# Kernel tuning notes

Hardware: AMD Instinct MI355X
Metric: run time of the kernel (lower is better)

The kernel has to match this reference:

```python
import jax, jax.numpy as jnp
import numpy as np

N = 12288
E = 196608
H = 128
Z = 128
NEG = -1e9  # finite mask value (avoids -inf NaNs in grads)
WSCALE = 0.05


def setup_inputs() -> dict:
    key = jax.random.key(0)
    ks = jax.random.split(key, 16)
    inp = {}
    inp["x"] = jax.random.normal(ks[0], (N, 2), dtype=jnp.float32)
    inp["z"] = jax.random.normal(ks[1], (Z,), dtype=jnp.float32)
    inp["node_type"] = jax.random.randint(ks[2], (N,), 0, 3, dtype=jnp.int32)
    inp["node_depth"] = jax.random.randint(ks[3], (N,), 0, 64, dtype=jnp.int32)
    inp["edge_index"] = jax.random.randint(ks[4], (2, E), 0, N, dtype=jnp.int32)
    inp["W1"] = jax.random.normal(ks[5], (2, H), dtype=jnp.float32) * WSCALE
    inp["b1"] = jnp.zeros((H,), jnp.float32)
    inp["W2"] = jax.random.normal(ks[6], (H, H), dtype=jnp.float32) * WSCALE
    inp["b2"] = jnp.zeros((H,), jnp.float32)
    inp["Wm1"] = jax.random.normal(ks[7], (H + Z, H), dtype=jnp.float32) * WSCALE
    inp["bm1"] = jnp.zeros((H,), jnp.float32)
    inp["Wm2"] = jax.random.normal(ks[8], (H, H), dtype=jnp.float32) * WSCALE
    inp["bm2"] = jnp.zeros((H,), jnp.float32)
    inp["Ws"] = jax.random.normal(ks[9], (H, H), dtype=jnp.float32) * WSCALE
    inp["Wt"] = jax.random.normal(ks[10], (H, H), dtype=jnp.float32) * WSCALE
    inp["Wi1"] = jax.random.normal(ks[11], (2 * H + Z, H), dtype=jnp.float32) * WSCALE
    inp["bi1"] = jnp.zeros((H,), jnp.float32)
    inp["Wi2"] = jax.random.normal(ks[12], (H, 1), dtype=jnp.float32) * WSCALE
    inp["bi2"] = jnp.zeros((1,), jnp.float32)
    return inp


def _gcn(x, W, b, src, dst, n):
    # GCNConv with self-loops and symmetric deg^-1/2 normalization
    loop = jnp.arange(n, dtype=src.dtype)
    s = jnp.concatenate([src, loop])
    d = jnp.concatenate([dst, loop])
    deg = jax.ops.segment_sum(jnp.ones_like(d, dtype=x.dtype), d, num_segments=n)
    inv_sqrt = jnp.where(deg > 0, jax.lax.rsqrt(jnp.maximum(deg, 1.0)), 0.0)
    w = inv_sqrt[s] * inv_sqrt[d]  # [E+N]
    agg = jax.ops.segment_sum(x[s] * w[:, None], d, num_segments=n)  # [N,F]
    return agg @ W + b


def reference(x, z, node_type, node_depth, edge_index,
              W1, b1, W2, b2, Wm1, bm1, Wm2, bm2, Ws, Wt, Wi1, bi1, Wi2, bi2):
    n = x.shape[0]
    src, dst = edge_index[0], edge_index[1]
    # 2-layer GCN encode
    h = jax.nn.relu(_gcn(x, W1, b1, src, dst, n))
    h = jax.nn.relu(_gcn(h, W2, b2, src, dst, n))
    # node_mlp on [h, z] (no outer relu, per original edge_index branch)
    zb = jnp.broadcast_to(z, (n, Z))
    h = jax.nn.relu(jnp.concatenate([h, zb], axis=1) @ Wm1 + bm1) @ Wm2 + bm2  # [N,H]
    # batched score: St[v,u] = tgt_proj(h_v) . src_proj(h_u)
    St = (h @ Wt) @ (h @ Ws).T  # [N(target), N(candidate)]
    cand_ok = node_depth[None, :] < node_depth[:, None]  # candidate strictly shallower
    St = jnp.where(cand_ok, St, NEG)
    vals, idx = jax.lax.top_k(St, 2)  # [N,2] per-target top candidates
    # target is active if type != 0, depth > 0, and at least one candidate exists
    tv = (node_type != 0) & (node_depth > 0) & (vals[:, 0] > NEG / 2)
    # k=2 edges for AND nodes (type==2), else k=1
    edge_valid = jnp.stack([tv, tv & (node_type == 2)], axis=1)  # [N,2]
    # inversion bit mlp on [h_u, h_v, z]
    hu = h[idx]  # [N,2,H]
    hv = jnp.broadcast_to(h[:, None, :], hu.shape)
    zz = jnp.broadcast_to(z, (n, 2, Z))
    feat = jnp.concatenate([hu, hv, zz], axis=-1)  # [N,2,2H+Z]
    logit = (jax.nn.relu(feat @ Wi1 + bi1) @ Wi2 + bi2)[..., 0]  # [N,2]
    inv_prob = jax.nn.sigmoid(logit)
    return inv_prob, vals, idx, edge_valid
```

## Files before the change

kernel.cpp:

```cpp
#include <hip/hip_runtime.h>
#include <hip/hip_bf16.h>

#define NN 12288
#define NE 196608
#define HD 128
#define ZD 128
#define NEGV (-1.0e9f)
#define SEG 16

using s8v = __attribute__((ext_vector_type(8))) short;
using f4v = __attribute__((ext_vector_type(4))) float;
using i4v = __attribute__((ext_vector_type(4))) int;

__device__ __forceinline__ unsigned short f2bf(float f) {
    return __builtin_bit_cast(unsigned short, __float2bfloat16(f));
}
__device__ __forceinline__ float4 pack8(float4 a, float4 b) {
    unsigned p0 = ((unsigned)f2bf(a.y) << 16) | f2bf(a.x);
    unsigned p1 = ((unsigned)f2bf(a.w) << 16) | f2bf(a.z);
    unsigned p2 = ((unsigned)f2bf(b.y) << 16) | f2bf(b.x);
    unsigned p3 = ((unsigned)f2bf(b.w) << 16) | f2bf(b.z);
    i4v r = (i4v){(int)p0, (int)p1, (int)p2, (int)p3};
    return __builtin_bit_cast(float4, r);
}

__global__ __launch_bounds__(256) void k_counts_wz(
        const int* __restrict__ edst, const int* __restrict__ ndep,
        const float* __restrict__ W2, const float* __restrict__ Wm1,
        const float* __restrict__ Wm2, const float* __restrict__ Wtm,
        const float* __restrict__ Wsm, const float* __restrict__ Wi1,
        const float* __restrict__ z, const float* __restrict__ bm1,
        const float* __restrict__ bi1,
        int* degi, int* cnt, __hip_bfloat16* __restrict__ wt7,
        float* cz1, float* cz2) {
    __shared__ int lh[64];
    int tid = threadIdx.x;
    int bid = blockIdx.x;
    if (bid < NE / 256) {
        int e = bid * 256 + tid;
        atomicAdd(&degi[edst[e]], 1);
    } else if (bid < NE / 256 + NN / 256) {
        if (tid < 64) lh[tid] = 0;
        __syncthreads();
        int v = (bid - NE / 256) * 256 + tid;
        atomicAdd(&lh[ndep[v]], 1);
        __syncthreads();
        if (tid < 64) {
            int c = lh[tid];
            if (c) atomicAdd(&cnt[tid * 16], c);
        }
    } else if (bid < NE / 256 + NN / 256 + 448) {
        int flat = (bid - NE / 256 - NN / 256) * 256 + tid;
        int g = flat >> 14;
        int rem = flat & 16383;
        int k = rem >> 7, n = rem & 127;
        const float* src;
        if (g == 0) src = W2;
        else if (g == 1) src = Wm1;
        else if (g == 2) src = Wm2;
        else if (g == 3) src = Wtm;
        else if (g == 4) src = Wsm;
        else if (g == 5) src = Wi1;
        else src = Wi1 + 128 * HD;
        wt7[(g << 14) + n * 128 + k] = __float2bfloat16(src[rem]);
    } else {
        int j = tid & 127;
        const float* W = (tid < 128) ? (Wm1 + HD * HD) : (Wi1 + 2 * HD * HD);
        float A0 = 0.f, A1 = 0.f, A2 = 0.f, A3 = 0.f;
        for (int k = 0; k < ZD; k += 4) {
            A0 = fmaf(z[k],     W[(k    ) * HD + j], A0);
            A1 = fmaf(z[k + 1], W[(k + 1) * HD + j], A1);
            A2 = fmaf(z[k + 2], W[(k + 2) * HD + j], A2);
            A3 = fmaf(z[k + 3], W[(k + 3) * HD + j], A3);
        }
        float r = (A0 + A1) + (A2 + A3);
        if (tid < 128) cz1[j] = r + bm1[j];
        else           cz2[j] = r + bi1[j];
    }
}

__global__ __launch_bounds__(1024) void k_prefix(const int* __restrict__ degi,
                                                 const int* __restrict__ cnt,
                                                 const float* __restrict__ x,
                                                 float* inv, float* agg2,
                                                 int* offs, int* cursor,
                                                 int* bofs, int* dcur) {
    __shared__ int ldeg[NN];
    __shared__ int part[1024];
    __shared__ int stot;
    int tid = threadIdx.x;
#pragma unroll
    for (int k = 0; k < 12; ++k)
        ldeg[k * 1024 + tid] = degi[k * 1024 + tid];
    __syncthreads();
    int base = tid * 12;
    int s = 0;
#pragma unroll
    for (int k = 0; k < 12; ++k) s += ldeg[base + k];
    part[tid] = s;
    __syncthreads();
    for (int off = 1; off < 1024; off <<= 1) {
        int v = (tid >= off) ? part[tid - off] : 0;
        __syncthreads();
        part[tid] += v;
        __syncthreads();
    }
    int run = part[tid] - s;
#pragma unroll
    for (int k = 0; k < 12; ++k) {
        int d = ldeg[base + k];
        ldeg[base + k] = run;
        run += d;
    }
    if (tid == 1023) stot = run;
    __syncthreads();
    int total = stot;
    const float2* X2 = (const float2*)x;
    float2* A2 = (float2*)agg2;
#pragma unroll
    for (int k = 0; k < 12; ++k) {
        int i = k * 1024 + tid;
        int p = ldeg[i];
        int nxt = (i < NN - 1) ? ldeg[i + 1] : total;
        int d = nxt - p;
        offs[i] = p;
        cursor[i] = p;
        float iv = rsqrtf((float)(d + 1));
        inv[i] = iv;
        float w = iv * iv;
        float2 xv = X2[i];
        float2 av; av.x = xv.x * w; av.y = xv.y * w;
        A2[i] = av;
    }
    if (tid == 0) {
        offs[NN] = total;
        int r = 0;
        for (int d = 0; d < 64; ++d) {
            bofs[d] = r;
            dcur[d * 16] = r;
            r += cnt[d * 16];
        }
        bofs[64] = r;
    }
}

__global__ __launch_bounds__(256) void k_bucket_scatter(
        const int* __restrict__ esrc, const int* __restrict__ edst,
        const int* __restrict__ ndep, const float* __restrict__ inv,
        int* cursor, int* ebsrc, float* ebw,
        int* dcur, int* sidx, int* sdep, int* prank) {
    __shared__ int lh[64];
    __shared__ int lbase[64];
    int tid = threadIdx.x;
    if (blockIdx.x < NE / 256) {
        int e = blockIdx.x * 256 + tid;
        int u = esrc[e], v = edst[e];
        int pos = atomicAdd(&cursor[v], 1);
        ebsrc[pos] = u;
        ebw[pos] = inv[u] * inv[v];
    } else {
        if (tid < 64) lh[tid] = 0;
        __syncthreads();
        int v = (blockIdx.x - NE / 256) * 256 + tid;
        int d = ndep[v];
        int r = atomicAdd(&lh[d], 1);
        __syncthreads();
        if (tid < 64) {
            int c = lh[tid];
            if (c) lbase[tid] = atomicAdd(&dcur[tid * 16], c);
        }
        __syncthreads();
        int p = lbase[d] + r;
        sidx[p] = v;
        sdep[p] = d;
        prank[v] = p;
    }
}

__global__ __launch_bounds__(256) void k_gl1(const int* __restrict__ offs,
                                             const int* __restrict__ ebsrc,
                                             const float* __restrict__ ebw,
                                             const float* __restrict__ x,
                                             const float* __restrict__ agg2,
                                             const float* __restrict__ W1,
                                             const float* __restrict__ b1,
                                             const float* __restrict__ inv,
                                             unsigned short* h1b, float* aggH) {
    __shared__ float2 la[32];
    int tid = threadIdx.x;
    int v0 = blockIdx.x * 32;
    {
        int nb = tid >> 3;
        int sl = tid & 7;
        int v = v0 + nb;
        int b = offs[v], e = offs[v + 1];
        const float2* X2 = (const float2*)x;
        float ax = 0.f, ay = 0.f;
        for (int k = b + sl; k < e; k += 8) {
            int u = ebsrc[k];
            float w = ebw[k];
            float2 xv = X2[u];
            ax = fmaf(xv.x, w, ax);
            ay = fmaf(xv.y, w, ay);
        }
#pragma unroll
        for (int m = 1; m < 8; m <<= 1) {
            ax += __shfl_xor(ax, m, 64);
            ay += __shfl_xor(ay, m, 64);
        }
        if (sl == 0) {
            float2 seed = ((const float2*)agg2)[v];
            seed.x += ax; seed.y += ay;
            la[nb] = seed;
        }
    }
    __syncthreads();
    {
#pragma unroll
        for (int k = 0; k < 16; ++k) {
            int idx = k * 256 + tid;
            int vloc = idx >> 7, j = idx & 127;
            float2 a = la[vloc];
            float hv = fmaxf(fmaf(a.x, W1[j], fmaf(a.y, W1[HD + j], b1[j])), 0.f);
            int t = (v0 + vloc) * HD + j;
            h1b[t] = f2bf(hv);
            float iv = inv[v0 + vloc];
            aggH[t] = hv * iv * iv;
        }
    }
}

__global__ __launch_bounds__(256) void k_gatherH(const int* __restrict__ offs,
                                                 const int* __restrict__ ebsrc,
                                                 const float* __restrict__ ebw,
                                                 const unsigned short* __restrict__ h1b,
                                                 float* aggH) {
    int tid = threadIdx.x;
    int lane = tid & 63;
    int v = blockIdx.x * 4 + (tid >> 6);
    const unsigned* H1 = (const unsigned*)h1b;
    float2* A2 = (float2*)aggH;
    float2 acc = A2[(size_t)v * 64 + lane];
    int b = offs[v], e = offs[v + 1];
    int k = b;
    for (; k + 4 <= e; k += 4) {
        int u0 = ebsrc[k], u1 = ebsrc[k + 1], u2 = ebsrc[k + 2], u3 = ebsrc[k + 3];
        float w0 = ebw[k], w1 = ebw[k + 1], w2 = ebw[k + 2], w3 = ebw[k + 3];
        unsigned hb0 = H1[(size_t)u0 * 64 + lane];
        unsigned hb1 = H1[(size_t)u1 * 64 + lane];
        unsigned hb2 = H1[(size_t)u2 * 64 + lane];
        unsigned hb3 = H1[(size_t)u3 * 64 + lane];
        acc.x = fmaf(__builtin_bit_cast(float, hb0 << 16), w0, acc.x);
        acc.y = fmaf(__builtin_bit_cast(float, hb0 & 0xFFFF0000u), w0, acc.y);
        acc.x = fmaf(__builtin_bit_cast(float, hb1 << 16), w1, acc.x);
        acc.y = fmaf(__builtin_bit_cast(float, hb1 & 0xFFFF0000u), w1, acc.y);
        acc.x = fmaf(__builtin_bit_cast(float, hb2 << 16), w2, acc.x);
        acc.y = fmaf(__builtin_bit_cast(float, hb2 & 0xFFFF0000u), w2, acc.y);
        acc.x = fmaf(__builtin_bit_cast(float, hb3 << 16), w3, acc.x);
        acc.y = fmaf(__builtin_bit_cast(float, hb3 & 0xFFFF0000u), w3, acc.y);
    }
    for (; k < e; ++k) {
        int u = ebsrc[k];
        float w = ebw[k];
        unsigned hb = H1[(size_t)u * 64 + lane];
        acc.x = fmaf(__builtin_bit_cast(float, hb << 16), w, acc.x);
        acc.y = fmaf(__builtin_bit_cast(float, hb & 0xFFFF0000u), w, acc.y);
    }
    A2[(size_t)v * 64 + lane] = acc;
}

#define AFRAGS(BUF) \
    s8v a0_ = __builtin_bit_cast(s8v, (BUF)[lane16 * 16 + ((quad     ) ^ lane16)]); \
    s8v a1_ = __builtin_bit_cast(s8v, (BUF)[lane16 * 16 + ((quad +  4) ^ lane16)]); \
    s8v a2_ = __builtin_bit_cast(s8v, (BUF)[lane16 * 16 + ((quad +  8) ^ lane16)]); \
    s8v a3_ = __builtin_bit_cast(s8v, (BUF)[lane16 * 16 + ((quad + 12) ^ lane16)]);

#define NBACC(WT4, NCOL, ACC) \
    f4v ACC = (f4v){0.f, 0.f, 0.f, 0.f}; \
    ACC = __builtin_amdgcn_mfma_f32_16x16x32_bf16(a0_, __builtin_bit_cast(s8v, (WT4)[(NCOL) * 16 + quad     ]), ACC, 0, 0, 0); \
    ACC = __builtin_amdgcn_mfma_f32_16x16x32_bf16(a1_, __builtin_bit_cast(s8v, (WT4)[(NCOL) * 16 + quad +  4]), ACC, 0, 0, 0); \
    ACC = __builtin_amdgcn_mfma_f32_16x16x32_bf16(a2_, __builtin_bit_cast(s8v, (WT4)[(NCOL) * 16 + quad +  8]), ACC, 0, 0, 0); \
    ACC = __builtin_amdgcn_mfma_f32_16x16x32_bf16(a3_, __builtin_bit_cast(s8v, (WT4)[(NCOL) * 16 + quad + 12]), ACC, 0, 0, 0);

#define BST(EXPR, RR, COL, USPTR) { int rw_ = quad * 4 + (RR); int cc_ = (COL) >> 3; \
    (USPTR)[rw_ * 128 + (((cc_ ^ rw_)) << 3) + ((COL) & 7)] = f2bf(EXPR); }

#define LDS4R(ACC, B, COL, US) \
    BST(fmaxf(ACC[0] + (B), 0.f), 0, COL, US) BST(fmaxf(ACC[1] + (B), 0.f), 1, COL, US) \
    BST(fmaxf(ACC[2] + (B), 0.f), 2, COL, US) BST(fmaxf(ACC[3] + (B), 0.f), 3, COL, US)

#define LDS4(ACC, B, COL, US) \
    BST(ACC[0] + (B), 0, COL, US) BST(ACC[1] + (B), 1, COL, US) \
    BST(ACC[2] + (B), 2, COL, US) BST(ACC[3] + (B), 3, COL, US)

#define GBF4S(ACC, COL, PTR) \
    ((unsigned short*)(PTR))[(size_t)pr0 * HD + (COL)] = f2bf(ACC[0]); \
    ((unsigned short*)(PTR))[(size_t)pr1 * HD + (COL)] = f2bf(ACC[1]); \
    ((unsigned short*)(PTR))[(size_t)pr2 * HD + (COL)] = f2bf(ACC[2]); \
    ((unsigned short*)(PTR))[(size_t)pr3 * HD + (COL)] = f2bf(ACC[3]);

#define GF4(ACC, B, COL, PTR) \
    (PTR)[(size_t)(r0 + quad * 4 + 0) * HD + (COL)] = ACC[0] + (B); \
    (PTR)[(size_t)(r0 + quad * 4 + 1) * HD + (COL)] = ACC[1] + (B); \
    (PTR)[(size_t)(r0 + quad * 4 + 2) * HD + (COL)] = ACC[2] + (B); \
    (PTR)[(size_t)(r0 + quad * 4 + 3) * HD + (COL)] = ACC[3] + (B);

__global__ __launch_bounds__(256) void k_mlp7_mfma(
        const float* __restrict__ s1in, const __hip_bfloat16* __restrict__ wt7,
        const float* __restrict__ bb2, const float* __restrict__ bcz1,
        const float* __restrict__ bbm2, const float* __restrict__ bcz2,
        const int* __restrict__ prank,
        float* __restrict__ outA, float* __restrict__ outB,
        __hip_bfloat16* __restrict__ htb, __hip_bfloat16* __restrict__ hsb) {
    __shared__ float4 bufA4[256];
    __shared__ float4 bufB4[256];
    int tid = threadIdx.x;
    int wv = tid >> 6;
    int l = tid & 63;
    int lane16 = l & 15;
    int quad = l >> 4;
    int r0 = blockIdx.x * 16;
    const float4* wt4 = (const float4*)wt7;

    int pr0 = prank[r0 + quad * 4 + 0];
    int pr1 = prank[r0 + quad * 4 + 1];
    int pr2 = prank[r0 + quad * 4 + 2];
    int pr3 = prank[r0 + quad * 4 + 3];

    {
        const float4* g4 = (const float4*)(s1in + (size_t)r0 * HD);
        float4 u0 = g4[2 * tid], u1 = g4[2 * tid + 1];
        int row_ = tid >> 4, c_ = tid & 15;
        bufA4[row_ * 16 + (c_ ^ row_)] = pack8(u0, u1);
    }
    __syncthreads();
    int col0 = wv * 32 + lane16, col1 = col0 + 16;
    unsigned short* usA = (unsigned short*)bufA4;
    unsigned short* usB = (unsigned short*)bufB4;

    {
        AFRAGS(bufA4)
        NBACC(wt4, col0, cA) NBACC(wt4, col1, cB)
        float q0 = bb2[col0], q1 = bb2[col1];
        LDS4R(cA, q0, col0, usB) LDS4R(cB, q1, col1, usB)
    }
    __syncthreads();
    {
        AFRAGS(bufB4)
        const float4* wt = wt4 + 2048;
        NBACC(wt, col0, cA) NBACC(wt, col1, cB)
        float q0 = bcz1[col0], q1 = bcz1[col1];
        LDS4R(cA, q0, col0, usA) LDS4R(cB, q1, col1, usA)
    }
    __syncthreads();
    {
        AFRAGS(bufA4)
        const float4* wt = wt4 + 2 * 2048;
        NBACC(wt, col0, cA) NBACC(wt, col1, cB)
        float q0 = bbm2[col0], q1 = bbm2[col1];
        LDS4(cA, q0, col0, usB) LDS4(cB, q1, col1, usB)
    }
    __syncthreads();
    {
        AFRAGS(bufB4)
        const float4* wt = wt4 + 3 * 2048;
        NBACC(wt, col0, cA) NBACC(wt, col1, cB)
        GBF4S(cA, col0, htb) GBF4S(cB, col1, htb)
    }
    {
        AFRAGS(bufB4)
        const float4* wt = wt4 + 4 * 2048;
        NBACC(wt, col0, cA) NBACC(wt, col1, cB)
        GBF4S(cA, col0, hsb) GBF4S(cB, col1, hsb)
    }
    {
        AFRAGS(bufB4)
        const float4* wt = wt4 + 5 * 2048;
        NBACC(wt, col0, cA) NBACC(wt, col1, cB)
        GF4(cA, 0.f, col0, outA) GF4(cB, 0.f, col1, outA)
    }
    {
        AFRAGS(bufB4)
        const float4* wt = wt4 + 6 * 2048;
        NBACC(wt, col0, cA) NBACC(wt, col1, cB)
        float q0 = bcz2[col0], q1 = bcz2[col1];
        GF4(cA, q0, col0, outB) GF4(cB, q1, col1, outB)
    }
}

#define STG(buf, q, val) { int r_ = (q) >> 4, c_ = (q) & 15; \
    (buf)[r_ * 16 + (c_ ^ (r_ & 7))] = (val); }

#define KC2(kc, AX, AY) { \
    int co_ = (kc) * 4 + quad; \
    int bo_ = bbase + (co_ ^ brm); \
    s8v b0_ = __builtin_bit_cast(s8v, B[bo_      ]); \
    s8v b1_ = __builtin_bit_cast(s8v, B[bo_ + 256]); \
    s8v b2_ = __builtin_bit_cast(s8v, B[bo_ + 512]); \
    s8v b3_ = __builtin_bit_cast(s8v, B[bo_ + 768]); \
    x0 = __builtin_amdgcn_mfma_f32_16x16x32_bf16(AX, b0_, x0, 0, 0, 0); \
    y0 = __builtin_amdgcn_mfma_f32_16x16x32_bf16(AY, b0_, y0, 0, 0, 0); \
    x1 = __builtin_amdgcn_mfma_f32_16x16x32_bf16(AX, b1_, x1, 0, 0, 0); \
    y1 = __builtin_amdgcn_mfma_f32_16x16x32_bf16(AY, b1_, y1, 0, 0, 0); \
    x2 = __builtin_amdgcn_mfma_f32_16x16x32_bf16(AX, b2_, x2, 0, 0, 0); \
    y2 = __builtin_amdgcn_mfma_f32_16x16x32_bf16(AY, b2_, y2, 0, 0, 0); \
    x3 = __builtin_amdgcn_mfma_f32_16x16x32_bf16(AX, b3_, x3, 0, 0, 0); \
    y3 = __builtin_amdgcn_mfma_f32_16x16x32_bf16(AY, b3_, y3, 0, 0, 0); }

#define RMG(K1, K2, EL, DV) { \
    unsigned pb_ = (__builtin_bit_cast(unsigned, EL) & 0xFFFFC000u) | e_; \
    float sf_ = __builtin_bit_cast(float, (du_ < (DV)) ? pb_ : negp_); \
    K2 = __builtin_amdgcn_fmed3f(K1, K2, sf_); \
    K1 = fmaxf(K1, sf_); }

#define MGEN(nb, XA, YA) { \
    unsigned pk_ = eds[ebase + (nb) * 16 + lane16]; \
    int du_ = (int)(pk_ >> 16); \
    unsigned e_ = pk_ & 0x3FFFu; \
    unsigned negp_ = negbase | e_; \
    RMG(k1x0, k2x0, XA[0], dvx0) RMG(k1x1, k2x1, XA[1], dvx1) \
    RMG(k1x2, k2x2, XA[2], dvx2) RMG(k1x3, k2x3, XA[3], dvx3) \
    RMG(k1y0, k2y0, YA[0], dvy0) RMG(k1y1, k2y1, YA[1], dvy1) \
    RMG(k1y2, k2y2, YA[2], dvy2) RMG(k1y3, k2y3, YA[3], dvy3) }

#define RMF(K1, K2, EL) { \
    float sf_ = __builtin_bit_cast(float, \
        (__builtin_bit_cast(unsigned, EL) & 0xFFFFC000u) | e_); \
    K2 = __builtin_amdgcn_fmed3f(K1, K2, sf_); \
    K1 = fmaxf(K1, sf_); }

#define MFAST(nb, XA, YA) { \
    unsigned e_ = eds[ebase + (nb) * 16 + lane16] & 0x3FFFu; \
    RMF(k1x0, k2x0, XA[0]) RMF(k1x1, k2x1, XA[1]) \
    RMF(k1x2, k2x2, XA[2]) RMF(k1x3, k2x3, XA[3]) \
    RMF(k1y0, k2y0, YA[0]) RMF(k1y1, k2y1, YA[1]) \
    RMF(k1y2, k2y2, YA[2]) RMF(k1y3, k2y3, YA[3]) }

#define BF1(K1, K2, m) { \
    float o1_ = __shfl_xor(K1, m, 64); \
    float o2_ = __shfl_xor(K2, m, 64); \
    float m2_ = fmaxf(K2, o2_); \
    K2 = __builtin_amdgcn_fmed3f(K1, o1_, m2_); \
    K1 = fmaxf(K1, o1_); }

#define BFALL(m) \
    BF1(k1x0, k2x0, m) BF1(k1x1, k2x1, m) BF1(k1x2, k2x2, m) BF1(k1x3, k2x3, m) \
    BF1(k1y0, k2y0, m) BF1(k1y1, k2y1, m) BF1(k1y2, k2y2, m) BF1(k1y3, k2y3, m)

#define EMIT2(K1, K2, GROW) { \
    size_t o = ((size_t)seg * NN + (GROW)) * 2; \
    pv[o] = K1; pv[o + 1] = K2; }

__global__ __launch_bounds__(256) void k_score_top2_mfma(
        const __hip_bfloat16* __restrict__ htb,
        const __hip_bfloat16* __restrict__ hsb,
        const int* __restrict__ sdep, const int* __restrict__ sidx,
        const int* __restrict__ bofs,
        float* __restrict__ pv) {
    __shared__ float4 Bs4[2][64 * 16];
    __shared__ unsigned eds[12 * 64];
    int tid = threadIdx.x;
    int w = tid >> 6;
    int l = tid & 63;
    int lane16 = l & 15;
    int quad = l >> 4;
    int rb = (int)gridDim.x - 1 - (int)blockIdx.x;
    int row0 = rb * 128;
    int seg = blockIdx.y;
    const unsigned negbase = __builtin_bit_cast(unsigned, NEGV) & 0xFFFFC000u;

    int dmax = sdep[row0 + 127];
    int lim = bofs[dmax];
    int nt = (lim + 63) >> 6;
    int ns = (nt + 11) / 12;
    if (ns < 1) ns = 1;
    if (seg >= ns) {
        if (tid < 128) {
            int grow = sidx[row0 + tid];
            size_t o = ((size_t)seg * NN + grow) * 2;
            pv[o]     = __builtin_bit_cast(float, negbase | 0x3FFFu);
            pv[o + 1] = __builtin_bit_cast(float, negbase | 0x3FFEu);
        }
        return;
    }
    int t0 = (seg * nt) / ns;
    int t1 = ((seg + 1) * nt) / ns;

    int rbase = row0 + w * 32;
    s8v ax0, ax1, ax2, ax3, ay0, ay1, ay2, ay3;
    {
        const float4* gx = (const float4*)(htb + (size_t)(rbase + lane16) * HD);
        ax0 = __builtin_bit_cast(s8v, gx[quad]);
        ax1 = __builtin_bit_cast(s8v, gx[4 + quad]);
        ax2 = __builtin_bit_cast(s8v, gx[8 + quad]);
        ax3 = __builtin_bit_cast(s8v, gx[12 + quad]);
        const float4* gy = (const float4*)(htb + (size_t)(rbase + 16 + lane16) * HD);
        ay0 = __builtin_bit_cast(s8v, gy[quad]);
        ay1 = __builtin_bit_cast(s8v, gy[4 + quad]);
        ay2 = __builtin_bit_cast(s8v, gy[8 + quad]);
        ay3 = __builtin_bit_cast(s8v, gy[12 + quad]);
    }
    for (int i = tid; i < (t1 - t0) * 64; i += 256) {
        int p = t0 * 64 + i;
        eds[i] = ((unsigned)sdep[p] << 16) | (0x3FFFu - (unsigned)sidx[p]);
    }
    if (t0 < t1) {
        float4* B0 = Bs4[t0 & 1];
        const float4* gb = (const float4*)(hsb + (size_t)(t0 * 64) * HD);
        float4 b0_ = gb[tid], b1_ = gb[tid + 256], b2_ = gb[tid + 512], b3_ = gb[tid + 768];
        STG(B0, tid, b0_) STG(B0, tid + 256, b1_)
        STG(B0, tid + 512, b2_) STG(B0, tid + 768, b3_)
    }

    int bbase = lane16 * 16, brm = lane16 & 7;

    int dvx0 = sdep[rbase + quad * 4 + 0];
    int dvx1 = sdep[rbase + quad * 4 + 1];
    int dvx2 = sdep[rbase + quad * 4 + 2];
    int dvx3 = sdep[rbase + quad * 4 + 3];
    int dvy0 = sdep[rbase + 16 + quad * 4 + 0];
    int dvy1 = sdep[rbase + 16 + quad * 4 + 1];
    int dvy2 = sdep[rbase + 16 + quad * 4 + 2];
    int dvy3 = sdep[rbase + 16 + quad * 4 + 3];
    int lim_lo = bofs[sdep[rbase]];
    int lim_hi = bofs[sdep[rbase + 31]];

    float ki1 = (lane16 == 0) ? __builtin_bit_cast(float, negbase | 0x3FFFu) : -3.4e38f;
    float ki2 = (lane16 == 0) ? __builtin_bit_cast(float, negbase | 0x3FFEu) : -3.4e38f;
    float k1x0 = ki1, k1x1 = ki1, k1x2 = ki1, k1x3 = ki1;
    float k1y0 = ki1, k1y1 = ki1, k1y2 = ki1, k1y3 = ki1;
    float k2x0 = ki2, k2x1 = ki2, k2x2 = ki2, k2x3 = ki2;
    float k2y0 = ki2, k2y1 = ki2, k2y2 = ki2, k2y3 = ki2;

    float4 p0, p1, p2, p3;
    for (int t = t0; t < t1; ++t) {
        int u0 = t * 64;
        int ebase = (t - t0) * 64;
        __syncthreads();
        if (t + 1 < t1) {
            const float4* g = (const float4*)(hsb + (size_t)(u0 + 64) * HD);
            p0 = g[tid]; p1 = g[tid + 256]; p2 = g[tid + 512]; p3 = g[tid + 768];
        }
        if (u0 < lim_hi) {
            const float4* B = Bs4[t & 1];
            f4v x0 = (f4v){0.f, 0.f, 0.f, 0.f};
            f4v x1 = (f4v){0.f, 0.f, 0.f, 0.f};
            f4v x2 = (f4v){0.f, 0.f, 0.f, 0.f};
            f4v x3 = (f4v){0.f, 0.f, 0.f, 0.f};
            f4v y0 = (f4v){0.f, 0.f, 0.f, 0.f};
            f4v y1 = (f4v){0.f, 0.f, 0.f, 0.f};
            f4v y2 = (f4v){0.f, 0.f, 0.f, 0.f};
            f4v y3 = (f4v){0.f, 0.f, 0.f, 0.f};
            KC2(0, ax0, ay0) KC2(1, ax1, ay1) KC2(2, ax2, ay2) KC2(3, ax3, ay3)
            if (u0 + 64 <= lim_lo) {
                MFAST(0, x0, y0) MFAST(1, x1, y1)
                MFAST(2, x2, y2) MFAST(3, x3, y3)
            } else {
                MGEN(0, x0, y0) MGEN(1, x1, y1)
                MGEN(2, x2, y2) MGEN(3, x3, y3)
            }
        }
        if (t + 1 < t1) {
            float4* Bn = Bs4[(t + 1) & 1];
            STG(Bn, tid, p0) STG(Bn, tid + 256, p1)
            STG(Bn, tid + 512, p2) STG(Bn, tid + 768, p3)
        }
    }

    BFALL(1) BFALL(2) BFALL(4) BFALL(8)

    if (lane16 == 0) {
        int gbse = rbase + quad * 4;
        EMIT2(k1x0, k2x0, sidx[gbse + 0])
        EMIT2(k1x1, k2x1, sidx[gbse + 1])
        EMIT2(k1x2, k2x2, sidx[gbse + 2])
        EMIT2(k1x3, k2x3, sidx[gbse + 3])
        EMIT2(k1y0, k2y0, sidx[gbse + 16])
        EMIT2(k1y1, k2y1, sidx[gbse + 17])
        EMIT2(k1y2, k2y2, sidx[gbse + 18])
        EMIT2(k1y3, k2y3, sidx[gbse + 19])
    }
}

__global__ __launch_bounds__(256) void k_final(const float* __restrict__ pv,
                                               const int* __restrict__ ntype,
                                               const int* __restrict__ ndepth,
                                               const float* __restrict__ A,
                                               const float* __restrict__ B,
                                               const float* __restrict__ Wi2,
                                               const float* __restrict__ bi2,
                                               float* __restrict__ out) {
    int tid = threadIdx.x;
    int lane = tid & 63;
    int v = blockIdx.x * 4 + (tid >> 6);

    float k1 = -3.4e38f;
    if (lane < 32) {
        k1 = pv[((size_t)(lane >> 1) * NN + v) * 2 + (lane & 1)];
    }
    float k2 = -3.4e38f;
#pragma unroll
    for (int m = 1; m <= 16; m <<= 1) {
        float o1 = __shfl_xor(k1, m, 64);
        float o2 = __shfl_xor(k2, m, 64);
        float m2 = fmaxf(k2, o2);
        k2 = __builtin_amdgcn_fmed3f(k1, o1, m2);
        k1 = fmaxf(k1, o1);
    }
    float K1 = __shfl(k1, 0, 64);
    float K2 = __shfl(k2, 0, 64);
    unsigned b1 = __builtin_bit_cast(unsigned, K1);
    unsigned b2 = __builtin_bit_cast(unsigned, K2);
    int I1 = 0x3FFF - (int)(b1 & 0x3FFFu);
    int I2 = 0x3FFF - (int)(b2 & 0x3FFFu);

    if (lane == 0) {
        int tp = ntype[v];
        bool tv = (tp != 0) && (ndepth[v] > 0) && (K1 > -5.0e8f);
        out[2 * NN + 2 * v]     = K1;
        out[2 * NN + 2 * v + 1] = K2;
        out[4 * NN + 2 * v]     = (float)I1;
        out[4 * NN + 2 * v + 1] = (float)I2;
        out[6 * NN + 2 * v]     = tv ? 1.f : 0.f;
        out[6 * NN + 2 * v + 1] = (tv && tp == 2) ? 1.f : 0.f;
    }

    int u1 = min(max(I1, 0), NN - 1);
    int u2 = min(max(I2, 0), NN - 1);
    const float2* A2p = (const float2*)A;
    float2 av1 = A2p[(size_t)u1 * 64 + lane];
    float2 av2 = A2p[(size_t)u2 * 64 + lane];
    float2 bv = ((const float2*)B)[(size_t)v * 64 + lane];
    float2 wv = ((const float2*)Wi2)[lane];
    float bias = bi2[0];
    float a1 = fmaf(fmaxf(av1.x + bv.x, 0.f), wv.x,
                    fmaxf(av1.y + bv.y, 0.f) * wv.y);
    float a2 = fmaf(fmaxf(av2.x + bv.x, 0.f), wv.x,
                    fmaxf(av2.y + bv.y, 0.f) * wv.y);
#pragma unroll
    for (int off = 32; off > 0; off >>= 1) {
        a1 += __shfl_down(a1, off);
        a2 += __shfl_down(a2, off);
    }
    if (lane == 0) {
        out[2 * v]     = 1.f / (1.f + expf(-(a1 + bias)));
        out[2 * v + 1] = 1.f / (1.f + expf(-(a2 + bias)));
    }
}

extern "C" void kernel_launch(void* const* d_in, const int* in_sizes, int n_in,
                              void* d_out, int out_size, void* d_ws, size_t ws_size,
                              hipStream_t stream) {
    (void)in_sizes; (void)n_in; (void)out_size; (void)ws_size;
    const float* x   = (const float*)d_in[0];
    const float* z   = (const float*)d_in[1];
    const int* ntype = (const int*)d_in[2];
    const int* ndep  = (const int*)d_in[3];
    const int* eidx  = (const int*)d_in[4];
    const float* W1  = (const float*)d_in[5];
    const float* b1  = (const float*)d_in[6];
    const float* W2  = (const float*)d_in[7];
    const float* b2  = (const float*)d_in[8];
    const float* Wm1 = (const float*)d_in[9];
    const float* bm1 = (const float*)d_in[10];
    const float* Wm2 = (const float*)d_in[11];
    const float* bm2 = (const float*)d_in[12];
    const float* Wsm = (const float*)d_in[13];
    const float* Wtm = (const float*)d_in[14];
    const float* Wi1 = (const float*)d_in[15];
    const float* bi1 = (const float*)d_in[16];
    const float* Wi2 = (const float*)d_in[17];
    const float* bi2 = (const float*)d_in[18];
    float* out = (float*)d_out;

    const int* esrc = eidx;
    const int* edst = eidx + NE;

    const size_t S2N = (size_t)SEG * 2 * NN;
    float* ws = (float*)d_ws;
    float* pv     = ws;
    int*   pi     = (int*)(pv + S2N);
    int*   cnt    = pi;
    int*   dcur   = pi + 1024;
    int*   degi   = pi + S2N;
    float* inv    = (float*)(degi + NN + 64);
    float* agg2   = inv + NN;
    float* cz1    = agg2 + 2 * NN;
    float* cz2    = cz1 + 128;
    int*   offs   = (int*)(cz2 + 128);
    int*   cursor = offs + NN + 16;
    int*   bofs   = cursor + NN;
    int*   sidx   = bofs + 80 + 64;
    int*   sdep   = sidx + NN;
    int*   prank  = sdep + NN;
    int*   ebsrc  = prank + NN;
    float* ebw    = (float*)(ebsrc + NE);
    __hip_bfloat16* wt7 = (__hip_bfloat16*)(ebw + NE);
    size_t F = (size_t)NN * HD;
    float* s0 = (float*)(wt7 + 7 * 16384);
    float* s1 = s0 + F;
    float* s2 = s1 + F;
    unsigned short* h1b = (unsigned short*)s0;
    __hip_bfloat16* htb = (__hip_bfloat16*)s0;
    __hip_bfloat16* hsb = htb + F;

    hipMemsetAsync(degi, 0, NN * sizeof(int), stream);
    hipMemsetAsync(cnt, 0, 1024 * sizeof(int), stream);
    k_counts_wz<<<NE / 256 + NN / 256 + 448 + 1, 256, 0, stream>>>(
        edst, ndep, W2, Wm1, Wm2, Wtm, Wsm, Wi1, z, bm1, bi1,
        degi, cnt, wt7, cz1, cz2);
    k_prefix<<<1, 1024, 0, stream>>>(degi, cnt, x, inv, agg2, offs, cursor, bofs, dcur);
    k_bucket_scatter<<<NE / 256 + NN / 256, 256, 0, stream>>>(
        esrc, edst, ndep, inv, cursor, ebsrc, ebw, dcur, sidx, sdep, prank);
    k_gl1<<<NN / 32, 256, 0, stream>>>(offs, ebsrc, ebw, x, agg2, W1, b1, inv,
                                       h1b, s1);
    k_gatherH<<<NN / 4, 256, 0, stream>>>(offs, ebsrc, ebw, h1b, s1);
    k_mlp7_mfma<<<NN / 16, 256, 0, stream>>>(s1, wt7, b2, cz1, bm2, cz2,
                                             prank, s2, s1, htb, hsb);
    k_score_top2_mfma<<<dim3(NN / 128, SEG), 256, 0, stream>>>(
        htb, hsb, sdep, sidx, bofs, pv);
    k_final<<<NN / 4, 256, 0, stream>>>(pv, ntype, ndep, s2, s1, Wi2, bi2, out);
}
```

Measured before the change: 225.6 us.

## Factor GCN edge weights into per-node scaling and transpose weights via shared memory

Removes the per-edge weight array by factoring the symmetric normalization: source features are pre-scaled by inv_sqrt (packed into an xi float4 and a pre-scaled bf16 h1), and the destination factor is applied once per node after the gather. This cuts the ebw writes in the scatter kernel and the ebw reads in both gather kernels. Separately, the weight transpose to bf16 now goes through a padded shared-memory tile, so both the reads and the writes are coalesced. In exchange the h1 values are rounded to bf16 after scaling, which shifts rounding slightly, and xi reuses the old ebw slot in the workspace.

```diff
diff --git a/kernel.cpp b/kernel.cpp
--- a/kernel.cpp
+++ b/kernel.cpp
@@ -34,6 +34,7 @@
         int* degi, int* cnt, __hip_bfloat16* __restrict__ wt7,
         float* cz1, float* cz2) {
     __shared__ int lh[64];
+    __shared__ float tl[16 * 129];
     int tid = threadIdx.x;
     int bid = blockIdx.x;
     if (bid < NE / 256) {
@@ -49,11 +50,10 @@
             int c = lh[tid];
             if (c) atomicAdd(&cnt[tid * 16], c);
         }
-    } else if (bid < NE / 256 + NN / 256 + 448) {
-        int flat = (bid - NE / 256 - NN / 256) * 256 + tid;
-        int g = flat >> 14;
-        int rem = flat & 16383;
-        int k = rem >> 7, n = rem & 127;
+    } else if (bid < NE / 256 + NN / 256 + 56) {
+        int b2 = bid - NE / 256 - NN / 256;
+        int g = b2 >> 3;
+        int k0 = (b2 & 7) << 4;
         const float* src;
         if (g == 0) src = W2;
         else if (g == 1) src = Wm1;
@@ -62,7 +62,19 @@
         else if (g == 4) src = Wsm;
         else if (g == 5) src = Wi1;
         else src = Wi1 + 128 * HD;
-        wt7[(g << 14) + n * 128 + k] = __float2bfloat16(src[rem]);
+#pragma unroll
+        for (int i = 0; i < 8; ++i) {
+            int idx = i * 256 + tid;
+            int kk = idx >> 7, n = idx & 127;
+            tl[kk * 129 + n] = src[(k0 + kk) * 128 + n];
+        }
+        __syncthreads();
+#pragma unroll
+        for (int i = 0; i < 8; ++i) {
+            int idx = i * 256 + tid;
+            int n = idx >> 4, kk = idx & 15;
+            wt7[(g << 14) + n * 128 + k0 + kk] = __float2bfloat16(tl[kk * 129 + n]);
+        }
     } else {
         int j = tid & 127;
         const float* W = (tid < 128) ? (Wm1 + HD * HD) : (Wi1 + 2 * HD * HD);
@@ -83,6 +95,7 @@
                                                  const int* __restrict__ cnt,
                                                  const float* __restrict__ x,
                                                  float* inv, float* agg2,
+                                                 float4* __restrict__ xi,
                                                  int* offs, int* cursor,
                                                  int* bofs, int* dcur) {
     __shared__ int ldeg[NN];
@@ -131,6 +144,8 @@
         float2 xv = X2[i];
         float2 av; av.x = xv.x * w; av.y = xv.y * w;
         A2[i] = av;
+        float4 xo; xo.x = xv.x; xo.y = xv.y; xo.z = iv; xo.w = 0.f;
+        xi[i] = xo;
     }
     if (tid == 0) {
         offs[NN] = total;
@@ -146,8 +161,8 @@
 
 __global__ __launch_bounds__(256) void k_bucket_scatter(
         const int* __restrict__ esrc, const int* __restrict__ edst,
-        const int* __restrict__ ndep, const float* __restrict__ inv,
-        int* cursor, int* ebsrc, float* ebw,
+        const int* __restrict__ ndep,
+        int* cursor, int* ebsrc,
         int* dcur, int* sidx, int* sdep, int* prank) {
     __shared__ int lh[64];
     __shared__ int lbase[64];
@@ -157,7 +172,6 @@
         int u = esrc[e], v = edst[e];
         int pos = atomicAdd(&cursor[v], 1);
         ebsrc[pos] = u;
-        ebw[pos] = inv[u] * inv[v];
     } else {
         if (tid < 64) lh[tid] = 0;
         __syncthreads();
@@ -179,8 +193,7 @@
 
 __global__ __launch_bounds__(256) void k_gl1(const int* __restrict__ offs,
                                              const int* __restrict__ ebsrc,
-                                             const float* __restrict__ ebw,
-                                             const float* __restrict__ x,
+                                             const float4* __restrict__ xi,
                                              const float* __restrict__ agg2,
                                              const float* __restrict__ W1,
                                              const float* __restrict__ b1,
@@ -194,14 +207,12 @@
         int sl = tid & 7;
         int v = v0 + nb;
         int b = offs[v], e = offs[v + 1];
-        const float2* X2 = (const float2*)x;
         float ax = 0.f, ay = 0.f;
         for (int k = b + sl; k < e; k += 8) {
             int u = ebsrc[k];
-            float w = ebw[k];
-            float2 xv = X2[u];
-            ax = fmaf(xv.x, w, ax);
-            ay = fmaf(xv.y, w, ay);
+            float4 xv = xi[u];
+            ax = fmaf(xv.x, xv.z, ax);
+            ay = fmaf(xv.y, xv.z, ay);
         }
 #pragma unroll
         for (int m = 1; m < 8; m <<= 1) {
@@ -209,8 +220,10 @@
             ay += __shfl_xor(ay, m, 64);
         }
         if (sl == 0) {
+            float ivv = inv[v];
             float2 seed = ((const float2*)agg2)[v];
-            seed.x += ax; seed.y += ay;
+            seed.x = fmaf(ax, ivv, seed.x);
+            seed.y = fmaf(ay, ivv, seed.y);
             la[nb] = seed;
         }
     }
@@ -223,8 +236,8 @@
             float2 a = la[vloc];
             float hv = fmaxf(fmaf(a.x, W1[j], fmaf(a.y, W1[HD + j], b1[j])), 0.f);
             int t = (v0 + vloc) * HD + j;
-            h1b[t] = f2bf(hv);
             float iv = inv[v0 + vloc];
+            h1b[t] = f2bf(hv * iv);
             aggH[t] = hv * iv * iv;
         }
     }
@@ -232,7 +245,7 @@
 
 __global__ __launch_bounds__(256) void k_gatherH(const int* __restrict__ offs,
                                                  const int* __restrict__ ebsrc,
-                                                 const float* __restrict__ ebw,
+                                                 const float* __restrict__ inv,
                                                  const unsigned short* __restrict__ h1b,
                                                  float* aggH) {
     int tid = threadIdx.x;
@@ -240,33 +253,35 @@
     int v = blockIdx.x * 4 + (tid >> 6);
     const unsigned* H1 = (const unsigned*)h1b;
     float2* A2 = (float2*)aggH;
-    float2 acc = A2[(size_t)v * 64 + lane];
+    float2 acc; acc.x = 0.f; acc.y = 0.f;
     int b = offs[v], e = offs[v + 1];
     int k = b;
     for (; k + 4 <= e; k += 4) {
         int u0 = ebsrc[k], u1 = ebsrc[k + 1], u2 = ebsrc[k + 2], u3 = ebsrc[k + 3];
-        float w0 = ebw[k], w1 = ebw[k + 1], w2 = ebw[k + 2], w3 = ebw[k + 3];
         unsigned hb0 = H1[(size_t)u0 * 64 + lane];
         unsigned hb1 = H1[(size_t)u1 * 64 + lane];
         unsigned hb2 = H1[(size_t)u2 * 64 + lane];
         unsigned hb3 = H1[(size_t)u3 * 64 + lane];
-        acc.x = fmaf(__builtin_bit_cast(float, hb0 << 16), w0, acc.x);
-        acc.y = fmaf(__builtin_bit_cast(float, hb0 & 0xFFFF0000u), w0, acc.y);
-        acc.x = fmaf(__builtin_bit_cast(float, hb1 << 16), w1, acc.x);
-        acc.y = fmaf(__builtin_bit_cast(float, hb1 & 0xFFFF0000u), w1, acc.y);
-        acc.x = fmaf(__builtin_bit_cast(float, hb2 << 16), w2, acc.x);
-        acc.y = fmaf(__builtin_bit_cast(float, hb2 & 0xFFFF0000u), w2, acc.y);
-        acc.x = fmaf(__builtin_bit_cast(float, hb3 << 16), w3, acc.x);
-        acc.y = fmaf(__builtin_bit_cast(float, hb3 & 0xFFFF0000u), w3, acc.y);
+        acc.x += __builtin_bit_cast(float, hb0 << 16);
+        acc.y += __builtin_bit_cast(float, hb0 & 0xFFFF0000u);
+        acc.x += __builtin_bit_cast(float, hb1 << 16);
+        acc.y += __builtin_bit_cast(float, hb1 & 0xFFFF0000u);
+        acc.x += __builtin_bit_cast(float, hb2 << 16);
+        acc.y += __builtin_bit_cast(float, hb2 & 0xFFFF0000u);
+        acc.x += __builtin_bit_cast(float, hb3 << 16);
+        acc.y += __builtin_bit_cast(float, hb3 & 0xFFFF0000u);
     }
     for (; k < e; ++k) {
         int u = ebsrc[k];
-        float w = ebw[k];
         unsigned hb = H1[(size_t)u * 64 + lane];
-        acc.x = fmaf(__builtin_bit_cast(float, hb << 16), w, acc.x);
-        acc.y = fmaf(__builtin_bit_cast(float, hb & 0xFFFF0000u), w, acc.y);
-    }
-    A2[(size_t)v * 64 + lane] = acc;
+        acc.x += __builtin_bit_cast(float, hb << 16);
+        acc.y += __builtin_bit_cast(float, hb & 0xFFFF0000u);
+    }
+    float ivv = inv[v];
+    float2 seed = A2[(size_t)v * 64 + lane];
+    seed.x = fmaf(acc.x, ivv, seed.x);
+    seed.y = fmaf(acc.y, ivv, seed.y);
+    A2[(size_t)v * 64 + lane] = seed;
 }
 
 #define AFRAGS(BUF) \
@@ -694,8 +709,9 @@
     int*   sdep   = sidx + NN;
     int*   prank  = sdep + NN;
     int*   ebsrc  = prank + NN;
-    float* ebw    = (float*)(ebsrc + NE);
-    __hip_bfloat16* wt7 = (__hip_bfloat16*)(ebw + NE);
+    float* ebwslot= (float*)(ebsrc + NE);
+    float4* xi    = (float4*)ebwslot;
+    __hip_bfloat16* wt7 = (__hip_bfloat16*)(ebwslot + NE);
     size_t F = (size_t)NN * HD;
     float* s0 = (float*)(wt7 + 7 * 16384);
     float* s1 = s0 + F;
@@ -706,15 +722,16 @@
 
     hipMemsetAsync(degi, 0, NN * sizeof(int), stream);
     hipMemsetAsync(cnt, 0, 1024 * sizeof(int), stream);
-    k_counts_wz<<<NE / 256 + NN / 256 + 448 + 1, 256, 0, stream>>>(
+    k_counts_wz<<<NE / 256 + NN / 256 + 56 + 1, 256, 0, stream>>>(
         edst, ndep, W2, Wm1, Wm2, Wtm, Wsm, Wi1, z, bm1, bi1,
         degi, cnt, wt7, cz1, cz2);
-    k_prefix<<<1, 1024, 0, stream>>>(degi, cnt, x, inv, agg2, offs, cursor, bofs, dcur);
+    k_prefix<<<1, 1024, 0, stream>>>(degi, cnt, x, inv, agg2, xi, offs, cursor,
+                                     bofs, dcur);
     k_bucket_scatter<<<NE / 256 + NN / 256, 256, 0, stream>>>(
-        esrc, edst, ndep, inv, cursor, ebsrc, ebw, dcur, sidx, sdep, prank);
-    k_gl1<<<NN / 32, 256, 0, stream>>>(offs, ebsrc, ebw, x, agg2, W1, b1, inv,
+        esrc, edst, ndep, cursor, ebsrc, dcur, sidx, sdep, prank);
+    k_gl1<<<NN / 32, 256, 0, stream>>>(offs, ebsrc, xi, agg2, W1, b1, inv,
                                        h1b, s1);
-    k_gatherH<<<NN / 4, 256, 0, stream>>>(offs, ebsrc, ebw, h1b, s1);
+    k_gatherH<<<NN / 4, 256, 0, stream>>>(offs, ebsrc, inv, h1b, s1);
     k_mlp7_mfma<<<NN / 16, 256, 0, stream>>>(s1, wt7, b2, cz1, bm2, cz2,
                                              prank, s2, s1, htb, hsb);
     k_score_top2_mfma<<<dim3(NN / 128, SEG), 256, 0, stream>>>(
```

Measured after the change: 224.8 us. About the same (-0.3%).
